# Kernel tuning notes

Hardware: AMD Instinct MI355X
Metric: run time of the kernel (lower is better)

## Reference

```python
import jax, jax.numpy as jnp
import numpy as np

T, B, D, H, R, O = 32, 8, 512, 512, 32, 512
CLIP_VAL = 1.0
LN_EPS = 1e-5


def setup_inputs() -> dict:
    key = jax.random.key(0)
    ks = jax.random.split(key, 8)
    rn = lambda k, sh, sc: (jax.random.normal(k, sh) * sc).astype(jnp.float32)
    inp = {
        'x': rn(ks[0], (T, B, D), 1.0),
        'h0': jnp.zeros((B, H), jnp.float32),
        'v0': jnp.zeros((B, H), jnp.float32),
        'dU0': jnp.zeros((B, H, H), jnp.float32),
        'trace_e0': jnp.zeros((B, H), jnp.float32),
        'trace_E0': jnp.zeros((B, H, H), jnp.float32),
        # parameters (init-scale approximations of the torch inits)
        'x2h_w': rn(ks[1], (2 * H, D), 1.0 / np.sqrt(D)),
        'x2h_b': jnp.zeros((2 * H,), jnp.float32),
        'h2h_w': rn(ks[2], (2 * H, H), 1.0 / np.sqrt(H)),
        'h2h_b': jnp.zeros((2 * H,), jnp.float32),
        'lnx_g': jnp.ones((2 * H,), jnp.float32),
        'lnx_b': jnp.zeros((2 * H,), jnp.float32),
        'lnh_g': jnp.ones((2 * H,), jnp.float32),
        'lnh_b': jnp.zeros((2 * H,), jnp.float32),
        'h2mod_w': rn(ks[3], (R, H), np.sqrt(2.0 / H)),
        'h2mod_b': jnp.zeros((R,), jnp.float32),
        'mod2h_w': rn(ks[4], (3, R), np.sqrt(2.0 / R)),
        'mod2h_b': jnp.zeros((3,), jnp.float32),
        'alpha': jnp.full((1,), -4.0, jnp.float32),
        'tau_U': jnp.full((1,), -4.5, jnp.float32),
        'dec_w': rn(ks[5], (O, H), 1.0 / np.sqrt(H)),
        'dec_b': jnp.zeros((O,), jnp.float32),
    }
    return inp


def _ln(y, g, b):
    mu = jnp.mean(y, axis=-1, keepdims=True)
    yc = y - mu
    var = jnp.mean(yc * yc, axis=-1, keepdims=True)
    return g * yc * jax.lax.rsqrt(var + LN_EPS) + b


def reference(x, h0, v0, dU0, trace_e0, trace_E0,
              x2h_w, x2h_b, h2h_w, h2h_b,
              lnx_g, lnx_b, lnh_g, lnh_b,
              h2mod_w, h2mod_b, mod2h_w, mod2h_b,
              alpha, tau_U, dec_w, dec_b):
    Hh = h0.shape[-1]
    sp_alpha = jax.nn.softplus(alpha)            # (1,)
    tau = jax.nn.sigmoid(tau_U)                  # (1,)
    # clip bounds derived from the candidate-row block of h2h weight
    w_dv = h2h_w[Hh:2 * Hh]                      # [H, H]
    upper = jax.nn.relu(CLIP_VAL - w_dv) / (sp_alpha + 1e-8)
    lower = -jax.nn.relu(CLIP_VAL + w_dv) / (sp_alpha + 1e-8)

    def step(carry, xt):
        h, v, dU, te, tE = carry
        Wx = _ln(xt @ x2h_w.T + x2h_b, lnx_g, lnx_b)           # [B, 2H]
        Wh = h @ h2h_w.T + h2h_b                               # [B, 2H]
        plast = sp_alpha * jnp.einsum('bij,bj->bi', dU, h)     # [B, H]
        Wh = Wh.at[:, Hh:].add(plast)
        Wh = _ln(Wh, lnh_g, lnh_b)
        z, dv = jnp.split(Wx + Wh, 2, axis=-1)
        z = jax.nn.sigmoid(z)
        v_n = (1.0 - z) * v + z * dv
        nh = jax.nn.relu(v_n)
        mod = jax.nn.relu(nh @ h2mod_w.T + h2mod_b) @ mod2h_w.T + mod2h_b  # [B, 3]
        r = jax.nn.sigmoid(mod[:, :1])                          # [B, 1]
        s = jax.nn.sigmoid(mod[:, 1])[:, None, None]            # [B, 1, 1]
        m = mod[:, 2][:, None, None]                            # [B, 1, 1]
        te_n = (1.0 - r) * te + r * h
        outer = nh[:, :, None] * te_n[:, None, :]               # [B, H, H]
        tE_n = (1.0 - s) * tE + s * (outer - jnp.swapaxes(outer, 1, 2))
        dU_n = (1.0 - tau) * dU + tau * m * tE_n
        dU_n = jnp.where(dU_n > upper, upper, dU_n)
        dU_n = jnp.where(dU_n < lower, lower, dU_n)
        return (nh, v_n, dU_n, te_n, tE_n), nh

    carry0 = (h0, v0, dU0, trace_e0, trace_E0)
    _, hs = jax.lax.scan(step, carry0, x)                        # hs: [T, B, H]
    out = hs @ dec_w.T + dec_b                                   # [T, B, O]
    return out
```

## Files before the change

### kernel.cpp

```cpp
#include <hip/hip_runtime.h>

#define TT 32
#define BB 8
#define DD 512
#define HH 512
#define RR 32
#define OO 512
#define H2 1024

typedef unsigned int uint;
typedef uint u32x4 __attribute__((ext_vector_type(4)));

#define OFF_WX    0
#define OFF_HS    262144
#define OFF_COLV  393216

#define HMW_P 528

__device__ __forceinline__ u32x4 ld16_coh(const u32x4* p) {
  u32x4 r;
  asm volatile("global_load_dwordx4 %0, %1, off sc0 sc1\n\ts_waitcnt vmcnt(0)"
               : "=v"(r) : "v"(p) : "memory");
  return r;
}
__device__ __forceinline__ void st16_coh(u32x4* p, u32x4 v) {
  asm volatile("global_store_dwordx4 %0, %1, off sc0 sc1"
               :: "v"(p), "v"(v) : "memory");
}
__device__ __forceinline__ float d4(const float4& a, const float4& b) {
  return a.x*b.x + a.y*b.y + a.z*b.z + a.w*b.w;
}

__global__ __launch_bounds__(512, 1) void sgru_persistent(
    const float* __restrict__ h0,     const float* __restrict__ v0,
    const float* __restrict__ dU0,    const float* __restrict__ tE0,
    const float* __restrict__ te0,
    const float* __restrict__ h2h_w,  const float* __restrict__ h2h_b,
    const float* __restrict__ lnh_g,  const float* __restrict__ lnh_b,
    const float* __restrict__ h2mod_w,const float* __restrict__ h2mod_b,
    const float* __restrict__ mod2h_w,const float* __restrict__ mod2h_b,
    const float* __restrict__ alpha_p,const float* __restrict__ tau_p,
    float* __restrict__ ws)
{
  const int tid = threadIdx.x;
  const int b   = blockIdx.x & 7;
  const int ir  = blockIdx.x >> 3;
  const int i0  = ir << 4;
  const int il  = tid >> 5;
  const int m   = tid & 31;
  const int gi  = i0 + il;

  const float* Wx = ws + OFF_WX;
  float* hsbuf    = ws + OFF_HS;
  u32x4* colvT    = (u32x4*)(ws + OFF_COLV);

  __shared__ float nh_s[2][HH];
  __shared__ float te_s[2][HH];
  __shared__ float hmw_s[RR * HMW_P];
  __shared__ float mp_s[RR];
  __shared__ float red_s[2][8];

  const float a_sp  = log1pf(__expf(alpha_p[0]));
  const float inv_a = 1.0f / (a_sp + 1e-8f);
  const float tau   = 1.0f / (1.0f + __expf(-tau_p[0]));
  const float c1t   = 1.0f - tau;

  float4 dUr[4], tEr[4], Wdvr[4], wlo[4], upr[4], lor[4];
  {
    const size_t rowoff = ((size_t)b * HH + gi) * HH;
    const size_t whioff = (size_t)(HH + gi) * HH;
    const size_t wlooff = (size_t)gi * HH;
#pragma unroll
    for (int q = 0; q < 4; ++q) {
      const int J = m + 32*q;
      dUr[q] = *reinterpret_cast<const float4*>(dU0 + rowoff + 4*J);
      tEr[q] = *reinterpret_cast<const float4*>(tE0 + rowoff + 4*J);
      wlo[q] = *reinterpret_cast<const float4*>(h2h_w + wlooff + 4*J);
      const float4 w = *reinterpret_cast<const float4*>(h2h_w + whioff + 4*J);
      Wdvr[q] = w;
      float4 u, l;
      u.x =  fmaxf(1.0f - w.x, 0.0f) * inv_a;  l.x = -fmaxf(1.0f + w.x, 0.0f) * inv_a;
      u.y =  fmaxf(1.0f - w.y, 0.0f) * inv_a;  l.y = -fmaxf(1.0f + w.y, 0.0f) * inv_a;
      u.z =  fmaxf(1.0f - w.z, 0.0f) * inv_a;  l.z = -fmaxf(1.0f + w.z, 0.0f) * inv_a;
      u.w =  fmaxf(1.0f - w.w, 0.0f) * inv_a;  l.w = -fmaxf(1.0f + w.w, 0.0f) * inv_a;
      upr[q] = u; lor[q] = l;
    }
  }

  const float rgz = lnh_g[tid],      rbz = lnh_b[tid];
  const float rgd = lnh_g[HH + tid], rbd = lnh_b[HH + tid];
  const float hbl = h2h_b[gi], hbh = h2h_b[HH + gi];
  const float hmb = h2mod_b[tid >> 4];
  const float mw0 = mod2h_w[tid & 31];
  const float mw1 = mod2h_w[RR + (tid & 31)];
  const float mw2 = mod2h_w[2*RR + (tid & 31)];
  const float mb0 = mod2h_b[0], mb1 = mod2h_b[1], mb2 = mod2h_b[2];
  float vreg = v0[b*HH + tid];

  nh_s[1][tid] = h0[b*HH + tid];
  te_s[0][tid] = te0[b*HH + tid];
  for (int idx = tid; idx < RR*HH; idx += 512)
    hmw_s[(idx >> 9)*HMW_P + (idx & 511)] = h2mod_w[idx];
  __syncthreads();

  {
    const float4* h4p = reinterpret_cast<const float4*>(nh_s[1]);
    float glo = 0.0f, gdv = 0.0f, plast = 0.0f;
#pragma unroll
    for (int q = 0; q < 4; ++q) {
      const float4 h4 = h4p[m + 32*q];
      glo   += d4(wlo[q],  h4);
      gdv   += d4(Wdvr[q], h4);
      plast += d4(dUr[q],  h4);
    }
#pragma unroll
    for (int off = 16; off >= 1; off >>= 1) {
      glo   += __shfl_xor(glo, off);
      gdv   += __shfl_xor(gdv, off);
      plast += __shfl_xor(plast, off);
    }
    if (m == 0) {
      u32x4 rec;
      rec.x = __float_as_uint(glo + hbl);
      rec.y = 1u;
      rec.z = __float_as_uint(gdv + hbh + a_sp*plast);
      rec.w = 1u;
      st16_coh(colvT + (size_t)(0*BB + b)*512 + gi, rec);
    }
  }

  float wxz = Wx[(size_t)(0*BB + b)*H2 + tid];
  float wxd = Wx[(size_t)(0*BB + b)*H2 + HH + tid];

  for (int t = 0; t < TT; ++t) {
    const int cur = t & 1;
    const uint want = (uint)(t + 1);

    const u32x4* p = colvT + (size_t)(cur*BB + b)*512 + tid;
    u32x4 r;
    for (;;) {
      r = ld16_coh(p);
      if (__all((r.y == want) & (r.w == want))) break;
      __builtin_amdgcn_s_sleep(2);
    }
    const float whz = __uint_as_float(r.x);
    const float whd = __uint_as_float(r.z);

    float s1 = whz + whd, s2 = whz*whz + whd*whd;
#pragma unroll
    for (int off = 32; off >= 1; off >>= 1) {
      s1 += __shfl_xor(s1, off);
      s2 += __shfl_xor(s2, off);
    }
    if ((tid & 63) == 0) { red_s[0][tid >> 6] = s1; red_s[1][tid >> 6] = s2; }
    __syncthreads();
    s1 = 0.0f; s2 = 0.0f;
#pragma unroll
    for (int w = 0; w < 8; ++w) { s1 += red_s[0][w]; s2 += red_s[1][w]; }
    const float mu   = s1 * (1.0f / H2);
    const float var  = s2 * (1.0f / H2) - mu * mu;
    const float rstd = rsqrtf(var + 1e-5f);

    const float yz = (whz - mu)*rstd*rgz + rbz + wxz;
    const float yd = (whd - mu)*rstd*rgd + rbd + wxd;
    const float z  = 1.0f / (1.0f + __expf(-yz));
    vreg = vreg + z * (yd - vreg);
    const float nh = fmaxf(vreg, 0.0f);
    nh_s[cur][tid] = nh;
    if (ir == 0) hsbuf[(size_t)(t*BB + b)*HH + tid] = nh;
    if (t == TT - 1) return;

    wxz = Wx[(size_t)((t+1)*BB + b)*H2 + tid];
    wxd = Wx[(size_t)((t+1)*BB + b)*H2 + HH + tid];
    __syncthreads();

    float glo = 0.0f, gdv = 0.0f;
    float4 h4q[4];
    {
      const float4* nh4 = reinterpret_cast<const float4*>(nh_s[cur]);
#pragma unroll
      for (int q = 0; q < 4; ++q) {
        h4q[q] = nh4[m + 32*q];
        glo += d4(wlo[q],  h4q[q]);
        gdv += d4(Wdvr[q], h4q[q]);
      }
#pragma unroll
      for (int off = 16; off >= 1; off >>= 1) {
        glo += __shfl_xor(glo, off);
        gdv += __shfl_xor(gdv, off);
      }
    }
    {
      const int rr = tid >> 4, kk = tid & 15;
      float part = 0.0f;
#pragma unroll
      for (int j = 0; j < 32; ++j)
        part += hmw_s[rr*HMW_P + kk + 16*j] * nh_s[cur][kk + 16*j];
#pragma unroll
      for (int off = 8; off >= 1; off >>= 1) part += __shfl_xor(part, off);
      if (kk == 0) mp_s[rr] = fmaxf(part + hmb, 0.0f);
    }
    __syncthreads();

    float r_b, s_b, c2t;
    {
      const float mp = mp_s[tid & 31];
      float a0 = mw0*mp, a1 = mw1*mp, a2 = mw2*mp;
#pragma unroll
      for (int off = 16; off >= 1; off >>= 1) {
        a0 += __shfl_xor(a0, off);
        a1 += __shfl_xor(a1, off);
        a2 += __shfl_xor(a2, off);
      }
      r_b = 1.0f / (1.0f + __expf(-(a0 + mb0)));
      s_b = 1.0f / (1.0f + __expf(-(a1 + mb1)));
      c2t = tau * (a2 + mb2);
    }

    {
      const float teo = te_s[cur][tid];
      te_s[1 - cur][tid] = teo + r_b * (nh_s[1 - cur][tid] - teo);
    }

    const float nh_i  = nh_s[cur][gi];
    const float teo_i = te_s[cur][gi];
    const float hp_i  = nh_s[1 - cur][gi];
    const float te_i  = teo_i + r_b * (hp_i - teo_i);
    float plast = 0.0f;
    {
      const float4* te4o = reinterpret_cast<const float4*>(te_s[cur]);
      const float4* hp4  = reinterpret_cast<const float4*>(nh_s[1 - cur]);
#pragma unroll
      for (int q = 0; q < 4; ++q) {
        const int J = m + 32*q;
        const float4 h4 = h4q[q];
        const float4 to = te4o[J];
        const float4 hp = hp4[J];
#define SGRU_UPD(C) { \
        float ten = to.C + r_b * (hp.C - to.C);              \
        float o   = nh_i * ten - h4.C * te_i;                \
        float tEn = tEr[q].C + s_b * (o - tEr[q].C);         \
        tEr[q].C  = tEn;                                                             \
        float d   = c1t * dUr[q].C + c2t * tEn;              \
        d = fminf(d, upr[q].C); d = fmaxf(d, lor[q].C);      \
        dUr[q].C  = d;                                                               \
        plast = fmaf(d, h4.C, plast); }
        SGRU_UPD(x) SGRU_UPD(y) SGRU_UPD(z) SGRU_UPD(w)
#undef SGRU_UPD
      }
#pragma unroll
      for (int off = 16; off >= 1; off >>= 1) plast += __shfl_xor(plast, off);
    }

    if (m == 0) {
      u32x4 rec;
      rec.x = __float_as_uint(glo + hbl);
      rec.y = (uint)(t + 2);
      rec.z = __float_as_uint(gdv + hbh + a_sp*plast);
      rec.w = (uint)(t + 2);
      st16_coh(colvT + (size_t)((1 - cur)*BB + b)*512 + gi, rec);
    }
  }
}

#define GBM 32
#define GBN 32
#define GBK 32
__global__ __launch_bounds__(256) void gemm_tn(
    const float* __restrict__ A, const float* __restrict__ W,
    const float* __restrict__ bias, float* __restrict__ C,
    int M, int N)
{
  const int K = 512;
  const int nbn = N / GBN;
  const int m0 = (blockIdx.x / nbn) * GBM;
  const int n0 = (blockIdx.x % nbn) * GBN;
  const int tid = threadIdx.x;
  const int tx = tid & 15;
  const int ty = tid >> 4;
  const int lr = tid >> 3;
  const int lc = tid & 7;
  __shared__ float As[GBK][36];
  __shared__ float Ws[GBK][36];
  float acc[2][2] = {};
  for (int kc = 0; kc < K; kc += GBK) {
    const float4 a0 = *reinterpret_cast<const float4*>(A + (size_t)(m0 + lr)*K + kc + lc*4);
    const float4 w0 = *reinterpret_cast<const float4*>(W + (size_t)(n0 + lr)*K + kc + lc*4);
    __syncthreads();
    As[lc*4+0][lr] = a0.x; As[lc*4+1][lr] = a0.y; As[lc*4+2][lr] = a0.z; As[lc*4+3][lr] = a0.w;
    Ws[lc*4+0][lr] = w0.x; Ws[lc*4+1][lr] = w0.y; Ws[lc*4+2][lr] = w0.z; Ws[lc*4+3][lr] = w0.w;
    __syncthreads();
#pragma unroll
    for (int k = 0; k < GBK; ++k) {
      const float2 am = *reinterpret_cast<const float2*>(&As[k][ty*2]);
      const float2 wn = *reinterpret_cast<const float2*>(&Ws[k][tx*2]);
      acc[0][0] += am.x*wn.x; acc[0][1] += am.x*wn.y;
      acc[1][0] += am.y*wn.x; acc[1][1] += am.y*wn.y;
    }
  }
  const float b0 = bias[n0 + tx*2], b1 = bias[n0 + tx*2 + 1];
  C[(size_t)(m0 + ty*2 + 0)*N + n0 + tx*2]     = acc[0][0] + b0;
  C[(size_t)(m0 + ty*2 + 0)*N + n0 + tx*2 + 1] = acc[0][1] + b1;
  C[(size_t)(m0 + ty*2 + 1)*N + n0 + tx*2]     = acc[1][0] + b0;
  C[(size_t)(m0 + ty*2 + 1)*N + n0 + tx*2 + 1] = acc[1][1] + b1;
}

__global__ __launch_bounds__(256) void ln_apply(
    float* __restrict__ Wp, const float* __restrict__ g, const float* __restrict__ b,
    u32x4* __restrict__ colvT)
{
  const int row = blockIdx.x;
  const int tid = threadIdx.x;
  {
    const int idx = row * 256 + tid;
    if (idx < 2*BB*512) {
      u32x4 z = {0u, 0u, 0u, 0u};
      colvT[idx] = z;
    }
  }
  float* rp = Wp + (size_t)row * H2;
  float4 v = *reinterpret_cast<const float4*>(rp + tid*4);
  float s1 = v.x + v.y + v.z + v.w;
  float s2 = v.x*v.x + v.y*v.y + v.z*v.z + v.w*v.w;
#pragma unroll
  for (int off = 32; off >= 1; off >>= 1) {
    s1 += __shfl_xor(s1, off);
    s2 += __shfl_xor(s2, off);
  }
  __shared__ float red[2][4];
  if ((tid & 63) == 0) { red[0][tid >> 6] = s1; red[1][tid >> 6] = s2; }
  __syncthreads();
  s1 = red[0][0] + red[0][1] + red[0][2] + red[0][3];
  s2 = red[1][0] + red[1][1] + red[1][2] + red[1][3];
  const float mu   = s1 * (1.0f / H2);
  const float var  = s2 * (1.0f / H2) - mu * mu;
  const float rstd = rsqrtf(var + 1e-5f);
  const float4 gv = *reinterpret_cast<const float4*>(g + tid*4);
  const float4 bv = *reinterpret_cast<const float4*>(b + tid*4);
  v.x = gv.x*(v.x - mu)*rstd + bv.x;
  v.y = gv.y*(v.y - mu)*rstd + bv.y;
  v.z = gv.z*(v.z - mu)*rstd + bv.z;
  v.w = gv.w*(v.w - mu)*rstd + bv.w;
  *reinterpret_cast<float4*>(rp + tid*4) = v;
}

extern "C" void kernel_launch(void* const* d_in, const int* in_sizes, int n_in,
                              void* d_out, int out_size, void* d_ws, size_t ws_size,
                              hipStream_t stream) {
  (void)in_sizes; (void)n_in; (void)out_size; (void)ws_size;
  const float* x        = (const float*)d_in[0];
  const float* h0       = (const float*)d_in[1];
  const float* v0       = (const float*)d_in[2];
  const float* dU0      = (const float*)d_in[3];
  const float* te0      = (const float*)d_in[4];
  const float* tE0      = (const float*)d_in[5];
  const float* x2h_w    = (const float*)d_in[6];
  const float* x2h_b    = (const float*)d_in[7];
  const float* h2h_w    = (const float*)d_in[8];
  const float* h2h_b    = (const float*)d_in[9];
  const float* lnx_g    = (const float*)d_in[10];
  const float* lnx_b    = (const float*)d_in[11];
  const float* lnh_g    = (const float*)d_in[12];
  const float* lnh_b    = (const float*)d_in[13];
  const float* h2mod_w  = (const float*)d_in[14];
  const float* h2mod_b  = (const float*)d_in[15];
  const float* mod2h_w  = (const float*)d_in[16];
  const float* mod2h_b  = (const float*)d_in[17];
  const float* alpha    = (const float*)d_in[18];
  const float* tau_U    = (const float*)d_in[19];
  const float* dec_w    = (const float*)d_in[20];
  const float* dec_b    = (const float*)d_in[21];

  float* ws = (float*)d_ws;

  gemm_tn<<<(TT*BB/GBM) * (H2/GBN), 256, 0, stream>>>(x, x2h_w, x2h_b,
                                                      ws + OFF_WX, TT*BB, H2);
  ln_apply<<<TT*BB, 256, 0, stream>>>(ws + OFF_WX, lnx_g, lnx_b,
                                      (u32x4*)(ws + OFF_COLV));

  sgru_persistent<<<256, 512, 0, stream>>>(h0, v0, dU0, tE0, te0,
                                           h2h_w, h2h_b, lnh_g, lnh_b,
                                           h2mod_w, h2mod_b, mod2h_w, mod2h_b,
                                           alpha, tau_U, ws);

  gemm_tn<<<(TT*BB/GBM) * (OO/GBN), 256, 0, stream>>>(ws + OFF_HS, dec_w, dec_b,
                                                      (float*)d_out, TT*BB, OO);
}
```

Before: 194.5 us.

## Replace per-element tagged records with per-block flag tags for step sync

The persistent recurrent kernel stops embedding a step tag inside each 16-byte data record. It now writes plain 8-byte value pairs, waits for its stores, syncs the block and then publishes one tag per producer block. Consumers poll 32 tags, one per producer, before doing a single load of the data. This halves the data traffic and shrinks polling, but adds a block barrier and a store drain on the critical path every step, plus a second dependent load after the poll.

```diff
diff --git a/kernel.cpp b/kernel.cpp
--- a/kernel.cpp
+++ b/kernel.cpp
@@ -9,23 +9,32 @@
 #define H2 1024
 
 typedef unsigned int uint;
-typedef uint u32x4 __attribute__((ext_vector_type(4)));
+typedef float f32x2 __attribute__((ext_vector_type(2)));
 
 #define OFF_WX    0
 #define OFF_HS    262144
 #define OFF_COLV  393216
+#define OFF_TAGS  409600
 
 #define HMW_P 528
 
-__device__ __forceinline__ u32x4 ld16_coh(const u32x4* p) {
-  u32x4 r;
-  asm volatile("global_load_dwordx4 %0, %1, off sc0 sc1\n\ts_waitcnt vmcnt(0)"
+__device__ __forceinline__ uint ld4_coh(const uint* p) {
+  uint r;
+  asm volatile("global_load_dword %0, %1, off sc0 sc1\n\ts_waitcnt vmcnt(0)"
                : "=v"(r) : "v"(p) : "memory");
   return r;
 }
-__device__ __forceinline__ void st16_coh(u32x4* p, u32x4 v) {
-  asm volatile("global_store_dwordx4 %0, %1, off sc0 sc1"
-               :: "v"(p), "v"(v) : "memory");
+__device__ __forceinline__ f32x2 ld8_coh(const f32x2* p) {
+  f32x2 r;
+  asm volatile("global_load_dwordx2 %0, %1, off sc0 sc1\n\ts_waitcnt vmcnt(0)"
+               : "=v"(r) : "v"(p) : "memory");
+  return r;
+}
+__device__ __forceinline__ void st8_coh(f32x2* p, f32x2 v) {
+  asm volatile("global_store_dwordx2 %0, %1, off sc0 sc1" :: "v"(p), "v"(v) : "memory");
+}
+__device__ __forceinline__ void st4_coh(uint* p, uint v) {
+  asm volatile("global_store_dword %0, %1, off sc0 sc1" :: "v"(p), "v"(v) : "memory");
 }
 __device__ __forceinline__ float d4(const float4& a, const float4& b) {
   return a.x*b.x + a.y*b.y + a.z*b.z + a.w*b.w;
@@ -52,7 +61,8 @@
 
   const float* Wx = ws + OFF_WX;
   float* hsbuf    = ws + OFF_HS;
-  u32x4* colvT    = (u32x4*)(ws + OFF_COLV);
+  f32x2* colvF    = (f32x2*)(ws + OFF_COLV);
+  uint*  tagsP    = (uint*)(ws + OFF_TAGS);
 
   __shared__ float nh_s[2][HH];
   __shared__ float te_s[2][HH];
@@ -120,13 +130,14 @@
       plast += __shfl_xor(plast, off);
     }
     if (m == 0) {
-      u32x4 rec;
-      rec.x = __float_as_uint(glo + hbl);
-      rec.y = 1u;
-      rec.z = __float_as_uint(gdv + hbh + a_sp*plast);
-      rec.w = 1u;
-      st16_coh(colvT + (size_t)(0*BB + b)*512 + gi, rec);
-    }
+      f32x2 rec;
+      rec.x = glo + hbl;
+      rec.y = gdv + hbh + a_sp*plast;
+      st8_coh(colvF + (size_t)(0*BB + b)*512 + gi, rec);
+    }
+    asm volatile("s_waitcnt vmcnt(0)" ::: "memory");
+    __syncthreads();
+    if (tid == 0) st4_coh(tagsP + (size_t)(0*BB + b)*32 + ir, 1u);
   }
 
   float wxz = Wx[(size_t)(0*BB + b)*H2 + tid];
@@ -136,15 +147,19 @@
     const int cur = t & 1;
     const uint want = (uint)(t + 1);
 
-    const u32x4* p = colvT + (size_t)(cur*BB + b)*512 + tid;
-    u32x4 r;
-    for (;;) {
-      r = ld16_coh(p);
-      if (__all((r.y == want) & (r.w == want))) break;
-      __builtin_amdgcn_s_sleep(2);
-    }
-    const float whz = __uint_as_float(r.x);
-    const float whd = __uint_as_float(r.z);
+    {
+      const uint* tg = tagsP + (size_t)(cur*BB + b)*32;
+      const int lane = tid & 63;
+      for (;;) {
+        uint v = want;
+        if (lane < 32) v = ld4_coh(tg + lane);
+        if (__all(v >= want)) break;
+        __builtin_amdgcn_s_sleep(1);
+      }
+    }
+    const f32x2 rec = ld8_coh(colvF + (size_t)(cur*BB + b)*512 + tid);
+    const float whz = rec.x;
+    const float whd = rec.y;
 
     float s1 = whz + whd, s2 = whz*whz + whd*whd;
 #pragma unroll
@@ -253,13 +268,14 @@
     }
 
     if (m == 0) {
-      u32x4 rec;
-      rec.x = __float_as_uint(glo + hbl);
-      rec.y = (uint)(t + 2);
-      rec.z = __float_as_uint(gdv + hbh + a_sp*plast);
-      rec.w = (uint)(t + 2);
-      st16_coh(colvT + (size_t)((1 - cur)*BB + b)*512 + gi, rec);
-    }
+      f32x2 rec2;
+      rec2.x = glo + hbl;
+      rec2.y = gdv + hbh + a_sp*plast;
+      st8_coh(colvF + (size_t)((1 - cur)*BB + b)*512 + gi, rec2);
+    }
+    asm volatile("s_waitcnt vmcnt(0)" ::: "memory");
+    __syncthreads();
+    if (tid == 0) st4_coh(tagsP + (size_t)((1 - cur)*BB + b)*32 + ir, (uint)(t + 2));
   }
 }
 
@@ -307,16 +323,13 @@
 
 __global__ __launch_bounds__(256) void ln_apply(
     float* __restrict__ Wp, const float* __restrict__ g, const float* __restrict__ b,
-    u32x4* __restrict__ colvT)
+    uint* __restrict__ tags)
 {
   const int row = blockIdx.x;
   const int tid = threadIdx.x;
-  {
-    const int idx = row * 256 + tid;
-    if (idx < 2*BB*512) {
-      u32x4 z = {0u, 0u, 0u, 0u};
-      colvT[idx] = z;
-    }
+  if (row == 0) {
+    tags[tid]       = 0u;
+    tags[tid + 256] = 0u;
   }
   float* rp = Wp + (size_t)row * H2;
   float4 v = *reinterpret_cast<const float4*>(rp + tid*4);
@@ -376,7 +389,7 @@
   gemm_tn<<<(TT*BB/GBM) * (H2/GBN), 256, 0, stream>>>(x, x2h_w, x2h_b,
                                                       ws + OFF_WX, TT*BB, H2);
   ln_apply<<<TT*BB, 256, 0, stream>>>(ws + OFF_WX, lnx_g, lnx_b,
-                                      (u32x4*)(ws + OFF_COLV));
+                                      (uint*)(ws + OFF_TAGS));
 
   sgru_persistent<<<256, 512, 0, stream>>>(h0, v0, dU0, tE0, te0,
                                            h2h_w, h2h_b, lnh_g, lnh_b,
```

After: 191.1 us. No clear change (-1.8%).
